# Kernel optimization log

Measured on AMD Instinct MI355X. Metric: run time of the kernel, lower is better.

## Reference

```python
import jax, jax.numpy as jnp
import numpy as np

VOCAB, EMB, HID = 32000, 512, 1024
B, T = 16, 128


def setup_inputs() -> dict:
    key = jax.random.key(0)
    ks = jax.random.split(key, 12)
    bound = 1.0 / np.sqrt(HID)
    u = lambda k, shape: jax.random.uniform(k, shape, jnp.float32, -bound, bound)
    return {
        "sentence": jax.random.randint(ks[0], (B, T), 0, VOCAB),
        "emb": jax.random.normal(ks[1], (VOCAB, EMB), jnp.float32),
        "W_i": u(ks[2], (EMB + HID, HID)), "b_i": u(ks[3], (HID,)),
        "W_f": u(ks[4], (EMB + HID, HID)), "b_f": u(ks[5], (HID,)),
        "W_o": u(ks[6], (EMB + HID, HID)), "b_o": u(ks[7], (HID,)),
        "W_c": u(ks[8], (EMB + HID, HID)), "b_c": u(ks[9], (HID,)),
        "W_hq": u(ks[10], (HID, VOCAB)), "b_q": u(ks[11], (VOCAB,)),
    }


def reference(sentence, emb, W_i, b_i, W_f, b_f, W_o, b_o, W_c, b_c, W_hq, b_q):
    # [B,T,E] -> [T,B,E]
    x = jnp.swapaxes(emb[sentence], 0, 1)
    # Fuse the 4 gate matmuls into one concatenated-weight matmul (same math).
    W = jnp.concatenate([W_i, W_f, W_o, W_c], axis=1)  # [E+H, 4H]
    b = jnp.concatenate([b_i, b_f, b_o, b_c])          # [4H]
    h0 = jnp.zeros((x.shape[1], HID), x.dtype)

    def step(carry, xt):
        h, c = carry
        z = jnp.concatenate([xt, h], axis=1) @ W + b   # [B,4H]
        i, f, o, g = jnp.split(z, 4, axis=1)
        i, f, o = jax.nn.sigmoid(i), jax.nn.sigmoid(f), jax.nn.sigmoid(o)
        c = f * c + i * jnp.tanh(g)
        h = o * jnp.tanh(c)
        return (h, c), h

    _, hs = jax.lax.scan(step, (h0, h0), x)            # [T,B,H]
    out = jnp.einsum('tbh,hv->tbv', hs, W_hq) + b_q    # [T,B,V]
    return jnp.transpose(out, (1, 2, 0))               # [B,V,T] as in torch permute(1,2,0)
```

## Files before the change

kernel.cpp:

```cpp
#include <hip/hip_runtime.h>
#include <math.h>

typedef float f32x4 __attribute__((ext_vector_type(4)));
typedef short bf16x8 __attribute__((ext_vector_type(8)));
typedef unsigned short u16;
typedef unsigned int u32;
typedef unsigned long long u64;

#define FLAG_STRIDE 16
#define FLAGS_TJ    8192
#define ACQ_BASE    8192
#define EPOCH_BASE  8448
#define FLAG_WORDS  ((EPOCH_BASE + 64) * FLAG_STRIDE)

__device__ __forceinline__ u16 f2bf(float f) {
    union { float f; unsigned u; } x; x.f = f;
    unsigned r = x.u + 0x7fff + ((x.u >> 16) & 1);
    return (u16)(r >> 16);
}

__device__ __forceinline__ void gload_lds16(const u16* g, u16* l) {
    __builtin_amdgcn_global_load_lds(
        (const __attribute__((address_space(1))) void*)g,
        (__attribute__((address_space(3))) void*)l, 16, 0, 0);
}

__global__ __launch_bounds__(256) void prep(
    const int* __restrict__ sent, const float* __restrict__ emb, u16* __restrict__ xb,
    const float* __restrict__ bi, const float* __restrict__ bf_,
    const float* __restrict__ bo, const float* __restrict__ bc, float* __restrict__ b4,
    const float* __restrict__ Wi, const float* __restrict__ Wf,
    const float* __restrict__ Wo, const float* __restrict__ Wc, u16* __restrict__ wxt,
    const float* __restrict__ Whq, u16* __restrict__ whqt) {
    __shared__ float tile[32][33];
    const int bx = blockIdx.x, tid = threadIdx.x;
    if (bx < 1024) {
        int row = bx * 2 + (tid >> 7);
        int t = row >> 4, b = row & 15;
        int idx = sent[b * 128 + t];
        float4 v = ((const float4*)(emb + (size_t)idx * 512))[tid & 127];
        ushort4 s = { f2bf(v.x), f2bf(v.y), f2bf(v.z), f2bf(v.w) };
        ((ushort4*)(xb + (size_t)row * 512))[tid & 127] = s;
        return;
    }
    if (bx < 1040) {
        int i = (bx - 1024) * 256 + tid;
        const float* p = (i < 1024) ? bi : (i < 2048) ? bf_ : (i < 3072) ? bo : bc;
        b4[i] = p[i & 1023];
        return;
    }
    const float* in; u16* out; int ldin, ldout, rt, ct;
    if (bx < 3088) {
        int q = bx - 1040, g = q >> 9, r = q & 511;
        in = (g == 0) ? Wi : (g == 1) ? Wf : (g == 2) ? Wo : Wc;
        ldin = 1024; out = wxt + (size_t)g * 1024 * 512; ldout = 512;
        rt = (r >> 5) * 32; ct = (r & 31) * 32;
    } else {
        int q = bx - 3088;
        in = Whq; ldin = 32000; out = whqt; ldout = 1024;
        rt = (q / 1000) * 32; ct = (q % 1000) * 32;
    }
    {
        int r = tid >> 3, cq = (tid & 7) * 4;
        float4 v = *(const float4*)(in + (size_t)(rt + r) * ldin + ct + cq);
        tile[r][cq] = v.x; tile[r][cq + 1] = v.y; tile[r][cq + 2] = v.z; tile[r][cq + 3] = v.w;
        __syncthreads();
        int c = tid >> 3, rq = (tid & 7) * 4;
        ushort4 s = { f2bf(tile[rq][c]), f2bf(tile[rq + 1][c]),
                      f2bf(tile[rq + 2][c]), f2bf(tile[rq + 3][c]) };
        *(ushort4*)(out + (size_t)(ct + c) * ldout + rt + rq) = s;
    }
}

__global__ __launch_bounds__(256) void gemm_xz(
    const u16* __restrict__ A, const u16* __restrict__ Bt,
    const float* __restrict__ bias, float* __restrict__ C) {
    const int tid = threadIdx.x;
    const int l = tid & 63, w = tid >> 6;
    const int wr = w >> 1, wc = w & 1;
    const int m0 = blockIdx.x * 128, n0 = blockIdx.y * 128;
    const int K = 512;
    __shared__ __align__(16) u16 As[128 * 64];
    __shared__ __align__(16) u16 Bs[128 * 64];
    f32x4 acc[4][4];
    f32x4 zz = { 0.f, 0.f, 0.f, 0.f };
#pragma unroll
    for (int i = 0; i < 4; i++)
#pragma unroll
        for (int j = 0; j < 4; j++) acc[i][j] = zz;
    for (int kt = 0; kt < (K >> 6); ++kt) {
        __syncthreads();
#pragma unroll
        for (int i = 0; i < 4; i++) {
            int cbase = i * 256 + w * 64;
            int c = cbase + l, row = c >> 3, kc = c & 7;
            gload_lds16(A + (size_t)(m0 + row) * K + kt * 64 + kc * 8, As + (size_t)cbase * 8);
            gload_lds16(Bt + (size_t)(n0 + row) * K + kt * 64 + kc * 8, Bs + (size_t)cbase * 8);
        }
        __syncthreads();
#pragma unroll
        for (int kk = 0; kk < 2; kk++) {
            bf16x8 af[4], bfv[4];
#pragma unroll
            for (int mi = 0; mi < 4; mi++)
                af[mi] = *(const bf16x8*)(As + (wr * 64 + mi * 16 + (l & 15)) * 64 + kk * 32 + (l >> 4) * 8);
#pragma unroll
            for (int ni = 0; ni < 4; ni++)
                bfv[ni] = *(const bf16x8*)(Bs + (wc * 64 + ni * 16 + (l & 15)) * 64 + kk * 32 + (l >> 4) * 8);
#pragma unroll
            for (int mi = 0; mi < 4; mi++)
#pragma unroll
                for (int ni = 0; ni < 4; ni++)
                    acc[mi][ni] = __builtin_amdgcn_mfma_f32_16x16x32_bf16(af[mi], bfv[ni], acc[mi][ni], 0, 0, 0);
        }
    }
    const int lr = l >> 4, lc = l & 15;
#pragma unroll
    for (int ni = 0; ni < 4; ni++) {
        int col = n0 + wc * 64 + ni * 16 + lc;
        float bv = bias[col];
#pragma unroll
        for (int mi = 0; mi < 4; mi++)
#pragma unroll
            for (int r = 0; r < 4; r++) {
                int row = m0 + wr * 64 + mi * 16 + lr * 4 + r;
                C[(size_t)row * 4096 + col] = acc[mi][ni][r] + bv;
            }
    }
}

__global__ __launch_bounds__(256, 1) void lstm_proj(
    u16* __restrict__ hs,
    const float* __restrict__ xz,
    const float* __restrict__ Wi, const float* __restrict__ Wf,
    const float* __restrict__ Wo, const float* __restrict__ Wc,
    u32* __restrict__ flags,
    const u16* __restrict__ whqt,
    const float* __restrict__ bq, float* __restrict__ out) {
    __shared__ __align__(16) char smem[37632];
    const int bx = blockIdx.x;
    const int tid = threadIdx.x;
    const int w = tid >> 6, l = tid & 63;

    if (tid == 0)
        __hip_atomic_fetch_add(&flags[(size_t)(ACQ_BASE + (bx & 255)) * FLAG_STRIDE], 0u,
                               __ATOMIC_ACQ_REL, __HIP_MEMORY_SCOPE_AGENT);

    if (bx < 64) {
        u16* hstage = (u16*)smem;
        float (*zlds)[16][17] = (float (*)[16][17])(void*)(smem + 32768);
        u32* lds_cnt = (u32*)(smem + 37120);
        const int j = bx;
        const int row = l & 15, hi = l >> 4;
        const float* Wg = (w == 0) ? Wi : (w == 1) ? Wf : (w == 2) ? Wo : Wc;
        if (tid == 0) *lds_cnt = 0;
        __builtin_amdgcn_s_setprio(1);

        bf16x8 wf[32];
#pragma unroll
        for (int kk = 0; kk < 32; ++kk)
#pragma unroll
            for (int e = 0; e < 8; ++e)
                wf[kk][e] = f2bf(Wg[(size_t)(512 + kk * 32 + hi * 8 + e) * 1024 + j * 16 + row]);
        __syncthreads();

        const int b = tid >> 4, hc = tid & 15;
        float cst = 0.f;
        const float* xr0 = xz + (size_t)b * 4096 + j * 16 + hc;
        float cz0 = xr0[0], cz1 = xr0[1024], cz2 = xr0[2048], cz3 = xr0[3072];

        for (int t = 0; t < 128; ++t) {
            if (t > 0) {
                if (w == 0) {
                    __builtin_amdgcn_s_setprio(0);
                    int spins = 0;
                    while (true) {
                        u32 f = __hip_atomic_load(&flags[(size_t)((t - 1) * 64 + l) * FLAG_STRIDE],
                                                  __ATOMIC_RELAXED, __HIP_MEMORY_SCOPE_SYSTEM);
                        if (__ballot(f != 0) == ~0ull) break;
                        __builtin_amdgcn_s_sleep(1);
                        if (++spins > (1 << 20)) break;
                    }
                    __builtin_amdgcn_s_setprio(1);
                    if (l == 0)
                        __hip_atomic_store(&flags[(size_t)(EPOCH_BASE + j) * FLAG_STRIDE], (u32)t,
                                           __ATOMIC_RELAXED, __HIP_MEMORY_SCOPE_SYSTEM);
                }
                __syncthreads();
                {
                    const u16* hbase = hs + (size_t)(t - 1) * 16 * 1024;
#pragma unroll
                    for (int q = 0; q < 8; ++q) {
                        int S = (w * 8 + q) * 64 + l;
                        int sr = S >> 7, ss = S & 127;
                        int c = (ss & ~7) | ((ss ^ sr) & 7);
                        gload_lds16(hbase + sr * 1024 + c * 8, hstage + (size_t)(w * 8 + q) * 512);
                    }
                }
            }
            float nz0 = 0.f, nz1 = 0.f, nz2 = 0.f, nz3 = 0.f;
            if (t < 127) {
                const float* xr = xz + (size_t)((t + 1) * 16 + b) * 4096 + j * 16 + hc;
                nz0 = xr[0]; nz1 = xr[1024]; nz2 = xr[2048]; nz3 = xr[3072];
            }
            if (t > 0) {
                __syncthreads();
                f32x4 zv = { 0.f, 0.f, 0.f, 0.f };
                f32x4 ac0 = zv, ac1 = zv, ac2 = zv, ac3 = zv;
#pragma unroll
                for (int kk = 0; kk < 32; kk += 4) {
#pragma unroll
                    for (int u = 0; u < 4; ++u) {
                        int c = (kk + u) * 4 + hi;
                        int s = (c & ~7) | ((c ^ row) & 7);
                        bf16x8 a = *(const bf16x8*)(hstage + row * 1024 + s * 8);
                        f32x4& ac = (u == 0) ? ac0 : (u == 1) ? ac1 : (u == 2) ? ac2 : ac3;
                        ac = __builtin_amdgcn_mfma_f32_16x16x32_bf16(a, wf[kk + u], ac, 0, 0, 0);
                    }
                }
                f32x4 acc = (ac0 + ac1) + (ac2 + ac3);
#pragma unroll
                for (int r = 0; r < 4; ++r)
                    zlds[w][hi * 4 + r][row] = acc[r];
            }
            __syncthreads();
            {
                float zi = cz0, zf = cz1, zo = cz2, zc = cz3;
                if (t > 0) {
                    zi += zlds[0][b][hc]; zf += zlds[1][b][hc];
                    zo += zlds[2][b][hc]; zc += zlds[3][b][hc];
                }
                float ig = 1.f / (1.f + __expf(-zi));
                float fg = 1.f / (1.f + __expf(-zf));
                float og = 1.f / (1.f + __expf(-zo));
                float gg = tanhf(zc);
                cst = fg * cst + ig * gg;
                float h = og * tanhf(cst);
                float hn = __shfl_xor(h, 1);
                if (!(l & 1)) {
                    unsigned pk = (unsigned)f2bf(h) | ((unsigned)f2bf(hn) << 16);
                    u32* dst = (u32*)hs + (((size_t)(t * 16 + b) * 1024 + j * 16 + hc) >> 1);
                    __hip_atomic_store(dst, pk, __ATOMIC_RELAXED, __HIP_MEMORY_SCOPE_SYSTEM);
                }
            }
            cz0 = nz0; cz1 = nz1; cz2 = nz2; cz3 = nz3;
            asm volatile("s_waitcnt vmcnt(0)" ::: "memory");
            if (l == 0) {
                u32 old = atomicAdd(lds_cnt, 1u);
                if (old == (u32)(4 * t + 3))
                    __hip_atomic_store(&flags[(size_t)(t * 64 + j) * FLAG_STRIDE], 1u,
                                       __ATOMIC_RELAXED, __HIP_MEMORY_SCOPE_SYSTEM);
            }
        }
        if (w == 0) {
            int spins = 0;
            while (true) {
                u32 f = __hip_atomic_load(&flags[(size_t)(127 * 64 + l) * FLAG_STRIDE],
                                          __ATOMIC_RELAXED, __HIP_MEMORY_SCOPE_SYSTEM);
                if (__ballot(f != 0) == ~0ull) break;
                __builtin_amdgcn_s_sleep(1);
                if (++spins > (1 << 20)) break;
            }
            if (l == 0)
                __hip_atomic_store(&flags[(size_t)(EPOCH_BASE + j) * FLAG_STRIDE], 128u,
                                   __ATOMIC_RELAXED, __HIP_MEMORY_SCOPE_SYSTEM);
        }
        return;
    }

    u16* As = (u16*)smem;
    u16* Bs = (u16*)(smem + 16384);
    const int pid = bx - 64;
    const int mchunk = pid / 250;
    const int n0 = (pid % 250) * 128;
    const int wr = w >> 1, wc = w & 1;

    if (w == 0) {
        const u32 need = (u32)(8 * mchunk + 8);
        int spins = 0;
        while (true) {
            u32 e = __hip_atomic_load(&flags[(size_t)(EPOCH_BASE + (pid & 63)) * FLAG_STRIDE],
                                      __ATOMIC_RELAXED, __HIP_MEMORY_SCOPE_SYSTEM);
            if (e >= need) break;
            __builtin_amdgcn_s_sleep(32);
            if (++spins > (1 << 17)) break;
        }
    }
    __syncthreads();

    f32x4 acc[4][4];
    f32x4 zz = { 0.f, 0.f, 0.f, 0.f };
#pragma unroll
    for (int i = 0; i < 4; i++)
#pragma unroll
        for (int jj = 0; jj < 4; jj++) acc[i][jj] = zz;

    const int K = 1024;
    for (int kt = 0; kt < 16; ++kt) {
        __syncthreads();
#pragma unroll
        for (int i = 0; i < 4; i++) {
            int cbase = i * 256 + w * 64;
            int c = cbase + l, row = c >> 3, kc = c & 7;
            int arow = (8 * mchunk + (row & 7)) * 16 + (row >> 3);
            gload_lds16(hs + (size_t)arow * K + kt * 64 + kc * 8, As + (size_t)cbase * 8);
            gload_lds16(whqt + (size_t)(n0 + row) * K + kt * 64 + kc * 8, Bs + (size_t)cbase * 8);
        }
        __syncthreads();
#pragma unroll
        for (int kk = 0; kk < 2; kk++) {
            bf16x8 af[4], bfv[4];
#pragma unroll
            for (int mi = 0; mi < 4; mi++)
                af[mi] = *(const bf16x8*)(As + (wr * 64 + mi * 16 + (l & 15)) * 64 + kk * 32 + (l >> 4) * 8);
#pragma unroll
            for (int ni = 0; ni < 4; ni++)
                bfv[ni] = *(const bf16x8*)(Bs + (wc * 64 + ni * 16 + (l & 15)) * 64 + kk * 32 + (l >> 4) * 8);
#pragma unroll
            for (int mi = 0; mi < 4; mi++)
#pragma unroll
                for (int ni = 0; ni < 4; ni++)
                    acc[mi][ni] = __builtin_amdgcn_mfma_f32_16x16x32_bf16(af[mi], bfv[ni], acc[mi][ni], 0, 0, 0);
        }
    }
    const int lr = l >> 4, lc = l & 15;
#pragma unroll
    for (int ni = 0; ni < 4; ni++) {
        int col = n0 + wc * 64 + ni * 16 + lc;
        float bv = bq[col];
#pragma unroll
        for (int mi = 0; mi < 4; mi++) {
            int r0 = wr * 64 + mi * 16 + lr * 4;
            int bb = r0 >> 3;
            int t0 = 8 * mchunk + (r0 & 7);
            float4 st = { acc[mi][ni][0] + bv, acc[mi][ni][1] + bv,
                          acc[mi][ni][2] + bv, acc[mi][ni][3] + bv };
            *(float4*)(out + (size_t)bb * 4096000 + (size_t)col * 128 + t0) = st;
        }
    }
}

extern "C" void kernel_launch(void* const* d_in, const int* in_sizes, int n_in,
                              void* d_out, int out_size, void* d_ws, size_t ws_size,
                              hipStream_t stream) {
    const int*   sent = (const int*)d_in[0];
    const float* emb  = (const float*)d_in[1];
    const float* W_i  = (const float*)d_in[2];
    const float* b_i  = (const float*)d_in[3];
    const float* W_f  = (const float*)d_in[4];
    const float* b_f  = (const float*)d_in[5];
    const float* W_o  = (const float*)d_in[6];
    const float* b_o  = (const float*)d_in[7];
    const float* W_c  = (const float*)d_in[8];
    const float* b_c  = (const float*)d_in[9];
    const float* W_hq = (const float*)d_in[10];
    const float* b_q  = (const float*)d_in[11];
    float* out = (float*)d_out;

    char* ws = (char*)d_ws;
    size_t off = 0;
    auto alloc = [&](size_t bytes) { void* p = ws + off; off += (bytes + 255) & ~255ull; return p; };
    u32*   flags = (u32*)alloc((size_t)FLAG_WORDS * 4);
    float* b4   = (float*)alloc((size_t)4096 * 4);
    u16*   xb   = (u16*)alloc((size_t)2048 * 512 * 2);
    u16*   wxt  = (u16*)alloc((size_t)4096 * 512 * 2);
    u16*   hs   = (u16*)alloc((size_t)2048 * 1024 * 2);
    float* xz   = (float*)alloc((size_t)2048 * 4096 * 4);
    u16*   whqt = (u16*)alloc((size_t)32000 * 1024 * 2);

    hipMemsetAsync(flags, 0, (size_t)FLAG_WORDS * 4, stream);
    prep<<<35088, 256, 0, stream>>>(sent, emb, xb, b_i, b_f, b_o, b_c, b4,
                                    W_i, W_f, W_o, W_c, wxt, W_hq, whqt);
    gemm_xz<<<dim3(16, 32), 256, 0, stream>>>(xb, wxt, b4, xz);
    lstm_proj<<<64 + 16 * 250, 256, 0, stream>>>(hs, xz, W_i, W_f, W_o, W_c,
                                                 flags, whqt, b_q, out);
}
```

Measured before the change: 773.0 us.

## Make projection blocks persistent, looping over timestep chunks and vocab tiles

The launch shrinks from 4064 one-shot blocks to 256. The 192 projection blocks each loop over all 16 timestep chunks and up to two vocab tiles, waiting on the recurrence epoch before each chunk. The LDS allocation grows to 96KB, likely so only one block fits per CU and the recurrence blocks are not starved. The s_setprio calls are also removed. Persistent blocks are meant to cut block-scheduling and spin-wait churn, and to let the output projection overlap the recurrence. The cost is less parallelism per chunk and possible load imbalance, since only 58 blocks get a second tile.

```diff
diff --git a/kernel.cpp b/kernel.cpp
--- a/kernel.cpp
+++ b/kernel.cpp
@@ -8,7 +8,6 @@
 typedef unsigned long long u64;
 
 #define FLAG_STRIDE 16
-#define FLAGS_TJ    8192
 #define ACQ_BASE    8192
 #define EPOCH_BASE  8448
 #define FLAG_WORDS  ((EPOCH_BASE + 64) * FLAG_STRIDE)
@@ -137,7 +136,7 @@
     u32* __restrict__ flags,
     const u16* __restrict__ whqt,
     const float* __restrict__ bq, float* __restrict__ out) {
-    __shared__ __align__(16) char smem[37632];
+    __shared__ __align__(16) char smem[98304];
     const int bx = blockIdx.x;
     const int tid = threadIdx.x;
     const int w = tid >> 6, l = tid & 63;
@@ -149,12 +148,11 @@
     if (bx < 64) {
         u16* hstage = (u16*)smem;
         float (*zlds)[16][17] = (float (*)[16][17])(void*)(smem + 32768);
-        u32* lds_cnt = (u32*)(smem + 37120);
+        u32* lds_cnt = (u32*)(smem + 37632);
         const int j = bx;
         const int row = l & 15, hi = l >> 4;
         const float* Wg = (w == 0) ? Wi : (w == 1) ? Wf : (w == 2) ? Wo : Wc;
         if (tid == 0) *lds_cnt = 0;
-        __builtin_amdgcn_s_setprio(1);
 
         bf16x8 wf[32];
 #pragma unroll
@@ -172,7 +170,6 @@
         for (int t = 0; t < 128; ++t) {
             if (t > 0) {
                 if (w == 0) {
-                    __builtin_amdgcn_s_setprio(0);
                     int spins = 0;
                     while (true) {
                         u32 f = __hip_atomic_load(&flags[(size_t)((t - 1) * 64 + l) * FLAG_STRIDE],
@@ -181,7 +178,6 @@
                         __builtin_amdgcn_s_sleep(1);
                         if (++spins > (1 << 20)) break;
                     }
-                    __builtin_amdgcn_s_setprio(1);
                     if (l == 0)
                         __hip_atomic_store(&flags[(size_t)(EPOCH_BASE + j) * FLAG_STRIDE], (u32)t,
                                            __ATOMIC_RELAXED, __HIP_MEMORY_SCOPE_SYSTEM);
@@ -270,72 +266,77 @@
 
     u16* As = (u16*)smem;
     u16* Bs = (u16*)(smem + 16384);
-    const int pid = bx - 64;
-    const int mchunk = pid / 250;
-    const int n0 = (pid % 250) * 128;
+    const int wid = bx - 64;
     const int wr = w >> 1, wc = w & 1;
-
-    if (w == 0) {
-        const u32 need = (u32)(8 * mchunk + 8);
-        int spins = 0;
-        while (true) {
-            u32 e = __hip_atomic_load(&flags[(size_t)(EPOCH_BASE + (pid & 63)) * FLAG_STRIDE],
-                                      __ATOMIC_RELAXED, __HIP_MEMORY_SCOPE_SYSTEM);
-            if (e >= need) break;
-            __builtin_amdgcn_s_sleep(32);
-            if (++spins > (1 << 17)) break;
-        }
-    }
-    __syncthreads();
-
-    f32x4 acc[4][4];
-    f32x4 zz = { 0.f, 0.f, 0.f, 0.f };
-#pragma unroll
-    for (int i = 0; i < 4; i++)
-#pragma unroll
-        for (int jj = 0; jj < 4; jj++) acc[i][jj] = zz;
-
-    const int K = 1024;
-    for (int kt = 0; kt < 16; ++kt) {
-        __syncthreads();
-#pragma unroll
-        for (int i = 0; i < 4; i++) {
-            int cbase = i * 256 + w * 64;
-            int c = cbase + l, row = c >> 3, kc = c & 7;
-            int arow = (8 * mchunk + (row & 7)) * 16 + (row >> 3);
-            gload_lds16(hs + (size_t)arow * K + kt * 64 + kc * 8, As + (size_t)cbase * 8);
-            gload_lds16(whqt + (size_t)(n0 + row) * K + kt * 64 + kc * 8, Bs + (size_t)cbase * 8);
-        }
-        __syncthreads();
-#pragma unroll
-        for (int kk = 0; kk < 2; kk++) {
-            bf16x8 af[4], bfv[4];
-#pragma unroll
-            for (int mi = 0; mi < 4; mi++)
-                af[mi] = *(const bf16x8*)(As + (wr * 64 + mi * 16 + (l & 15)) * 64 + kk * 32 + (l >> 4) * 8);
-#pragma unroll
-            for (int ni = 0; ni < 4; ni++)
-                bfv[ni] = *(const bf16x8*)(Bs + (wc * 64 + ni * 16 + (l & 15)) * 64 + kk * 32 + (l >> 4) * 8);
-#pragma unroll
-            for (int mi = 0; mi < 4; mi++)
-#pragma unroll
-                for (int ni = 0; ni < 4; ni++)
-                    acc[mi][ni] = __builtin_amdgcn_mfma_f32_16x16x32_bf16(af[mi], bfv[ni], acc[mi][ni], 0, 0, 0);
-        }
-    }
     const int lr = l >> 4, lc = l & 15;
-#pragma unroll
-    for (int ni = 0; ni < 4; ni++) {
-        int col = n0 + wc * 64 + ni * 16 + lc;
-        float bv = bq[col];
-#pragma unroll
-        for (int mi = 0; mi < 4; mi++) {
-            int r0 = wr * 64 + mi * 16 + lr * 4;
-            int bb = r0 >> 3;
-            int t0 = 8 * mchunk + (r0 & 7);
-            float4 st = { acc[mi][ni][0] + bv, acc[mi][ni][1] + bv,
-                          acc[mi][ni][2] + bv, acc[mi][ni][3] + bv };
-            *(float4*)(out + (size_t)bb * 4096000 + (size_t)col * 128 + t0) = st;
+
+    for (int m = 0; m < 16; ++m) {
+        if (w == 0) {
+            const u32 need = (u32)(8 * m + 8);
+            int spins = 0;
+            while (true) {
+                u32 e = __hip_atomic_load(&flags[(size_t)(EPOCH_BASE + (wid & 63)) * FLAG_STRIDE],
+                                          __ATOMIC_RELAXED, __HIP_MEMORY_SCOPE_SYSTEM);
+                if (e >= need) break;
+                __builtin_amdgcn_s_sleep(16);
+                if (++spins > (1 << 18)) break;
+            }
+        }
+        __syncthreads();
+
+        for (int nn = 0; nn < 2; ++nn) {
+            int nt = wid + nn * 192;
+            if (nt >= 250) break;
+            const int n0 = nt * 128;
+            f32x4 acc[4][4];
+            f32x4 zz = { 0.f, 0.f, 0.f, 0.f };
+#pragma unroll
+            for (int i = 0; i < 4; i++)
+#pragma unroll
+                for (int jj = 0; jj < 4; jj++) acc[i][jj] = zz;
+
+            for (int kt = 0; kt < 16; ++kt) {
+                __syncthreads();
+#pragma unroll
+                for (int i = 0; i < 4; i++) {
+                    int cbase = i * 256 + w * 64;
+                    int c = cbase + l, rowi = c >> 3, kc = c & 7;
+                    int arow = (8 * m + (rowi & 7)) * 16 + (rowi >> 3);
+                    gload_lds16(hs + (size_t)arow * 1024 + kt * 64 + kc * 8, As + (size_t)cbase * 8);
+                    gload_lds16(whqt + (size_t)(n0 + rowi) * 1024 + kt * 64 + kc * 8, Bs + (size_t)cbase * 8);
+                }
+                __syncthreads();
+#pragma unroll
+                for (int kk = 0; kk < 2; kk++) {
+                    bf16x8 af[4], bfv[4];
+#pragma unroll
+                    for (int mi = 0; mi < 4; mi++)
+                        af[mi] = *(const bf16x8*)(As + (wr * 64 + mi * 16 + lc) * 64 + kk * 32 + lr * 8);
+#pragma unroll
+                    for (int ni = 0; ni < 4; ni++)
+                        bfv[ni] = *(const bf16x8*)(Bs + (wc * 64 + ni * 16 + lc) * 64 + kk * 32 + lr * 8);
+#pragma unroll
+                    for (int mi = 0; mi < 4; mi++)
+#pragma unroll
+                        for (int ni = 0; ni < 4; ni++)
+                            acc[mi][ni] = __builtin_amdgcn_mfma_f32_16x16x32_bf16(af[mi], bfv[ni], acc[mi][ni], 0, 0, 0);
+                }
+            }
+#pragma unroll
+            for (int ni = 0; ni < 4; ni++) {
+                int col = n0 + wc * 64 + ni * 16 + lc;
+                float bv = bq[col];
+#pragma unroll
+                for (int mi = 0; mi < 4; mi++) {
+                    int r0 = wr * 64 + mi * 16 + lr * 4;
+                    int bb = r0 >> 3;
+                    int t0 = 8 * m + (r0 & 7);
+                    float4 st = { acc[mi][ni][0] + bv, acc[mi][ni][1] + bv,
+                                  acc[mi][ni][2] + bv, acc[mi][ni][3] + bv };
+                    *(float4*)(out + (size_t)bb * 4096000 + (size_t)col * 128 + t0) = st;
+                }
+            }
+            __syncthreads();
         }
     }
 }
@@ -372,6 +373,6 @@
     prep<<<35088, 256, 0, stream>>>(sent, emb, xb, b_i, b_f, b_o, b_c, b4,
                                     W_i, W_f, W_o, W_c, wxt, W_hq, whqt);
     gemm_xz<<<dim3(16, 32), 256, 0, stream>>>(xb, wxt, b4, xz);
-    lstm_proj<<<64 + 16 * 250, 256, 0, stream>>>(hs, xz, W_i, W_f, W_o, W_c,
-                                                 flags, whqt, b_q, out);
-}
+    lstm_proj<<<256, 256, 0, stream>>>(hs, xz, W_i, W_f, W_o, W_c,
+                                       flags, whqt, b_q, out);
+}
```

After: 870.5 us. 1.13x slower.
